# Kernel optimization log

Hardware: AMD Instinct MI355X
Metric: run time of the kernel (lower is better)

The kernel has to match this reference:

```python
import jax, jax.numpy as jnp
import numpy as np

K = 3          # kernel_size
P = K // 2     # padding


def setup_inputs() -> dict:
    key = jax.random.key(0)
    # [B, C, H, W]; first C-4 channels are per-class probabilities, last 4 are box offsets
    points = jax.random.normal(key, (4, 84, 512, 512), dtype=jnp.float32)
    return {"points": points}


def reference(points):
    # Peak (point) NMS: keep a pixel iff torch.argmax over its KxK window of
    # max-class-probability lands exactly on the window center.
    # torch.argmax returns the FIRST flat index attaining the max, so the center
    # survives iff it is strictly greater than every earlier (row-major) window
    # element and >= every later element.
    probs = jnp.max(points[:, :-4], axis=1)            # [B, H, W]
    B, H, W = probs.shape
    padded = jnp.pad(probs, ((0, 0), (P, P), (P, P)))  # zero pad, matches F.pad default
    center_idx = P * K + P
    mask = jnp.ones((B, H, W), dtype=bool)
    for di in range(K):                                # small fixed K*K loop (8 iters)
        for dj in range(K):
            idx = di * K + dj
            if idx == center_idx:
                continue
            nb = padded[:, di:di + H, dj:dj + W]       # neighbor value at this offset
            cmp = (probs > nb) if idx < center_idx else (probs >= nb)
            mask = mask & cmp
    # non-peaks zeroed across ALL channels, exactly like the zeros_like + scatter
    return points * mask[:, None, :, :].astype(points.dtype)
```

## Files before the change

### kernel.cpp

```cpp
#include <hip/hip_runtime.h>

#define BB 4
#define CC 84
#define CM 80
#define HH 512
#define WW 512
#define HWSZ (HH * WW)
#define PG (HWSZ / 4)
#define NCH 4
#define CPC (CM / NCH)

typedef float v4f __attribute__((ext_vector_type(4)));

static __device__ __forceinline__ v4f vmax4(v4f a, v4f b) {
    v4f r;
    r.x = fmaxf(a.x, b.x);
    r.y = fmaxf(a.y, b.y);
    r.z = fmaxf(a.z, b.z);
    r.w = fmaxf(a.w, b.w);
    return r;
}

__global__ __launch_bounds__(256) void partial_max_kernel(const float* __restrict__ pts,
                                                          float* __restrict__ partial) {
    int tid = blockIdx.x * blockDim.x + threadIdx.x;
    int pg  = tid & (PG - 1);
    int r   = tid >> 16;
    int chunk = r % NCH;
    int b     = r / NCH;

    const v4f* base = (const v4f*)pts + ((size_t)b * CC + chunk * CPC) * PG + pg;
    v4f m = __builtin_nontemporal_load(base);
#pragma unroll 5
    for (int c = 1; c < CPC; ++c) {
        v4f v = __builtin_nontemporal_load(base + (size_t)c * PG);
        m = vmax4(m, v);
    }
    ((v4f*)partial)[((size_t)chunk * BB + b) * PG + pg] = m;
}

__global__ __launch_bounds__(256) void fused_mask_kernel(const float* __restrict__ partial,
                                                         float* __restrict__ mask) {
    int tid = blockIdx.x * blockDim.x + threadIdx.x;
    int pg  = tid & (PG - 1);
    int b   = tid >> 16;
    int off = pg << 2;
    int h   = off >> 9;
    int w0  = off & (WW - 1);

    float rows[3][6];
#pragma unroll
    for (int r = 0; r < 3; ++r) {
        int hh = h + r - 1;
        bool hv = (hh >= 0) & (hh < HH);
#pragma unroll
        for (int ci = 0; ci < 6; ++ci) {
            int ww = w0 + ci - 1;
            bool wv = (ww >= 0) & (ww < WW);
            float v = 0.0f;
            if (hv & wv) {
                int pidx = hh * WW + ww;
                v = partial[(size_t)(0 * BB + b) * HWSZ + pidx];
#pragma unroll
                for (int ch = 1; ch < NCH; ++ch)
                    v = fmaxf(v, partial[(size_t)(ch * BB + b) * HWSZ + pidx]);
            }
            rows[r][ci] = v;
        }
    }

    v4f fm;
#pragma unroll
    for (int j = 0; j < 4; ++j) {
        float v = rows[1][j + 1];
        bool m = (v >  rows[0][j]) & (v >  rows[0][j + 1]) & (v >  rows[0][j + 2])
               & (v >  rows[1][j]) & (v >= rows[1][j + 2])
               & (v >= rows[2][j]) & (v >= rows[2][j + 1]) & (v >= rows[2][j + 2]);
        float f = m ? 1.0f : 0.0f;
        if (j == 0) fm.x = f;
        else if (j == 1) fm.y = f;
        else if (j == 2) fm.z = f;
        else fm.w = f;
    }
    ((v4f*)mask)[(size_t)b * PG + pg] = fm;
}

__global__ __launch_bounds__(256) void mul_kernel(const float* __restrict__ pts,
                                                  const float* __restrict__ mask,
                                                  float* __restrict__ out) {
    int gid = blockIdx.x;
    int c   = gid % CC;
    int pc  = gid / CC;
    int b   = pc >> 8;
    int pg  = ((pc & 255) << 8) + threadIdx.x;

    v4f m = ((const v4f*)mask)[(size_t)b * PG + pg];
    size_t idx = ((size_t)b * CC + c) * PG + pg;

    unsigned nz = (__float_as_uint(m.x) | __float_as_uint(m.y) |
                   __float_as_uint(m.z) | __float_as_uint(m.w));
    v4f o;
    if (nz) {
        v4f v = __builtin_nontemporal_load((const v4f*)pts + idx);
        o.x = v.x * m.x;
        o.y = v.y * m.y;
        o.z = v.z * m.z;
        o.w = v.w * m.w;
    } else {
        o.x = 0.f; o.y = 0.f; o.z = 0.f; o.w = 0.f;
    }
    __builtin_nontemporal_store(o, (v4f*)out + idx);
}

__global__ __launch_bounds__(256) void probs_kernel_fb(const float* __restrict__ pts,
                                                       float* __restrict__ probs) {
    int tid = blockIdx.x * blockDim.x + threadIdx.x;
    int pix = tid << 2;
    int b   = pix >> 18;
    int off = pix & (HWSZ - 1);
    const float4* base = (const float4*)(pts + (size_t)b * CC * HWSZ + off);
    float4 m = base[0];
#pragma unroll 4
    for (int c = 1; c < CM; ++c) {
        float4 v = base[c * (HWSZ / 4)];
        m.x = fmaxf(m.x, v.x); m.y = fmaxf(m.y, v.y);
        m.z = fmaxf(m.z, v.z); m.w = fmaxf(m.w, v.w);
    }
    ((float4*)probs)[tid] = m;
}

__global__ __launch_bounds__(256) void nms_mul_kernel_fb(const float* __restrict__ pts,
                                                         const float* __restrict__ probs,
                                                         float* __restrict__ out) {
    int tid = blockIdx.x * blockDim.x + threadIdx.x;
    int pix = tid << 2;
    int b   = pix >> 18;
    int off = pix & (HWSZ - 1);
    int h   = off >> 9;
    int w0  = off & (WW - 1);
    const float* pb = probs + b * HWSZ;
    float rows[3][6];
#pragma unroll
    for (int r = 0; r < 3; ++r) {
        int hh = h + r - 1;
        bool hv = (hh >= 0) & (hh < HH);
        const float* rp = pb + hh * WW;
#pragma unroll
        for (int ci = 0; ci < 6; ++ci) {
            int ww = w0 + ci - 1;
            bool wv = (ww >= 0) & (ww < WW);
            rows[r][ci] = (hv & wv) ? rp[ww] : 0.0f;
        }
    }
    float fm[4];
    bool any = false;
#pragma unroll
    for (int j = 0; j < 4; ++j) {
        float v = rows[1][j + 1];
        bool m = (v >  rows[0][j]) & (v >  rows[0][j + 1]) & (v >  rows[0][j + 2])
               & (v >  rows[1][j]) & (v >= rows[1][j + 2])
               & (v >= rows[2][j]) & (v >= rows[2][j + 1]) & (v >= rows[2][j + 2]);
        fm[j] = m ? 1.0f : 0.0f;
        any |= m;
    }
    size_t bo = (size_t)b * CC * HWSZ + off;
    const float4* src = (const float4*)(pts + bo);
    float4* dst = (float4*)(out + bo);
    if (any) {
#pragma unroll 4
        for (int c = 0; c < CC; ++c) {
            float4 v = src[c * (HWSZ / 4)];
            float4 o;
            o.x = v.x * fm[0]; o.y = v.y * fm[1];
            o.z = v.z * fm[2]; o.w = v.w * fm[3];
            dst[c * (HWSZ / 4)] = o;
        }
    } else {
        float4 z = make_float4(0.f, 0.f, 0.f, 0.f);
#pragma unroll 4
        for (int c = 0; c < CC; ++c) dst[c * (HWSZ / 4)] = z;
    }
}

extern "C" void kernel_launch(void* const* d_in, const int* in_sizes, int n_in,
                              void* d_out, int out_size, void* d_ws, size_t ws_size,
                              hipStream_t stream) {
    const float* pts = (const float*)d_in[0];
    float* out = (float*)d_out;
    float* ws  = (float*)d_ws;

    const size_t MB4 = (size_t)BB * HWSZ * sizeof(float);
    dim3 blk(256);
    dim3 grd_pg(BB * PG / 256);

    if (ws_size >= (NCH + 1) * MB4) {
        float* partial = ws;
        float* mask    = ws + (size_t)NCH * BB * HWSZ;
        partial_max_kernel<<<dim3(BB * NCH * PG / 256), blk, 0, stream>>>(pts, partial);
        fused_mask_kernel<<<grd_pg, blk, 0, stream>>>(partial, mask);
        mul_kernel<<<dim3(BB * CC * (PG / 256)), blk, 0, stream>>>(pts, mask, out);
    } else {
        float* probs = ws;
        probs_kernel_fb<<<grd_pg, blk, 0, stream>>>(pts, probs);
        nms_mul_kernel_fb<<<grd_pg, blk, 0, stream>>>(pts, probs, out);
    }
}
```

Baseline: 614.7 us.

## Fuse mask and multiply into one kernel; halve partial-max channel splits

Merges the stencil mask kernel and the per-channel multiply kernel into one kernel. Each block now computes the 3x3 peak mask itself and then streams 42 channels of points to the output, so the mask buffer is no longer written and re-read. The partial-max stage now splits channels into 2 chunks instead of 4, which shrinks the partial buffer and the stencil's reads. In exchange, the stencil is recomputed twice per pixel (once per half), and each thread runs a long serial channel loop with fewer blocks in flight.

```diff
diff --git a/kernel.cpp b/kernel.cpp
--- a/kernel.cpp
+++ b/kernel.cpp
@@ -7,8 +7,9 @@
 #define WW 512
 #define HWSZ (HH * WW)
 #define PG (HWSZ / 4)
-#define NCH 4
-#define CPC (CM / NCH)
+#define SPL 2
+#define CPS (CM / SPL)
+#define CPB (CC / SPL)
 
 typedef float v4f __attribute__((ext_vector_type(4)));
 
@@ -26,27 +27,33 @@
     int tid = blockIdx.x * blockDim.x + threadIdx.x;
     int pg  = tid & (PG - 1);
     int r   = tid >> 16;
-    int chunk = r % NCH;
-    int b     = r / NCH;
-
-    const v4f* base = (const v4f*)pts + ((size_t)b * CC + chunk * CPC) * PG + pg;
+    int half = r & 1;
+    int b    = r >> 1;
+
+    const v4f* base = (const v4f*)pts + ((size_t)b * CC + half * CPS) * PG + pg;
     v4f m = __builtin_nontemporal_load(base);
-#pragma unroll 5
-    for (int c = 1; c < CPC; ++c) {
+#pragma unroll 8
+    for (int c = 1; c < CPS; ++c) {
         v4f v = __builtin_nontemporal_load(base + (size_t)c * PG);
         m = vmax4(m, v);
     }
-    ((v4f*)partial)[((size_t)chunk * BB + b) * PG + pg] = m;
-}
-
-__global__ __launch_bounds__(256) void fused_mask_kernel(const float* __restrict__ partial,
-                                                         float* __restrict__ mask) {
-    int tid = blockIdx.x * blockDim.x + threadIdx.x;
-    int pg  = tid & (PG - 1);
-    int b   = tid >> 16;
-    int off = pg << 2;
-    int h   = off >> 9;
-    int w0  = off & (WW - 1);
+    ((v4f*)partial)[((size_t)half * BB + b) * PG + pg] = m;
+}
+
+__global__ __launch_bounds__(256) void nms_mul_kernel(const float* __restrict__ pts,
+                                                      const float* __restrict__ partial,
+                                                      float* __restrict__ out) {
+    int gid  = blockIdx.x;
+    int half = gid & 1;
+    int pc   = gid >> 1;
+    int b    = pc >> 8;
+    int pg   = ((pc & 255) << 8) + threadIdx.x;
+    int off  = pg << 2;
+    int h    = off >> 9;
+    int w0   = off & (WW - 1);
+
+    const float* p0 = partial + (size_t)b * HWSZ;
+    const float* p1 = partial + ((size_t)BB + b) * HWSZ;
 
     float rows[3][6];
 #pragma unroll
@@ -60,10 +67,7 @@
             float v = 0.0f;
             if (hv & wv) {
                 int pidx = hh * WW + ww;
-                v = partial[(size_t)(0 * BB + b) * HWSZ + pidx];
-#pragma unroll
-                for (int ch = 1; ch < NCH; ++ch)
-                    v = fmaxf(v, partial[(size_t)(ch * BB + b) * HWSZ + pidx]);
+                v = fmaxf(p0[pidx], p1[pidx]);
             }
             rows[r][ci] = v;
         }
@@ -82,34 +86,30 @@
         else if (j == 2) fm.z = f;
         else fm.w = f;
     }
-    ((v4f*)mask)[(size_t)b * PG + pg] = fm;
-}
-
-__global__ __launch_bounds__(256) void mul_kernel(const float* __restrict__ pts,
-                                                  const float* __restrict__ mask,
-                                                  float* __restrict__ out) {
-    int gid = blockIdx.x;
-    int c   = gid % CC;
-    int pc  = gid / CC;
-    int b   = pc >> 8;
-    int pg  = ((pc & 255) << 8) + threadIdx.x;
-
-    v4f m = ((const v4f*)mask)[(size_t)b * PG + pg];
-    size_t idx = ((size_t)b * CC + c) * PG + pg;
-
-    unsigned nz = (__float_as_uint(m.x) | __float_as_uint(m.y) |
-                   __float_as_uint(m.z) | __float_as_uint(m.w));
-    v4f o;
+    unsigned nz = (__float_as_uint(fm.x) | __float_as_uint(fm.y) |
+                   __float_as_uint(fm.z) | __float_as_uint(fm.w));
+
+    const v4f* src = (const v4f*)pts + ((size_t)b * CC + half * CPB) * PG + pg;
+    v4f*       dst = (v4f*)out       + ((size_t)b * CC + half * CPB) * PG + pg;
+
     if (nz) {
-        v4f v = __builtin_nontemporal_load((const v4f*)pts + idx);
-        o.x = v.x * m.x;
-        o.y = v.y * m.y;
-        o.z = v.z * m.z;
-        o.w = v.w * m.w;
+#pragma unroll 6
+        for (int c = 0; c < CPB; ++c) {
+            v4f v = __builtin_nontemporal_load(src + (size_t)c * PG);
+            v4f o;
+            o.x = v.x * fm.x;
+            o.y = v.y * fm.y;
+            o.z = v.z * fm.z;
+            o.w = v.w * fm.w;
+            __builtin_nontemporal_store(o, dst + (size_t)c * PG);
+        }
     } else {
-        o.x = 0.f; o.y = 0.f; o.z = 0.f; o.w = 0.f;
-    }
-    __builtin_nontemporal_store(o, (v4f*)out + idx);
+        v4f z;
+        z.x = 0.0f; z.y = 0.0f; z.z = 0.0f; z.w = 0.0f;
+#pragma unroll 6
+        for (int c = 0; c < CPB; ++c)
+            __builtin_nontemporal_store(z, dst + (size_t)c * PG);
+    }
 }
 
 __global__ __launch_bounds__(256) void probs_kernel_fb(const float* __restrict__ pts,
@@ -189,18 +189,16 @@
     float* out = (float*)d_out;
     float* ws  = (float*)d_ws;
 
-    const size_t MB4 = (size_t)BB * HWSZ * sizeof(float);
+    const size_t PSZ = (size_t)SPL * BB * HWSZ * sizeof(float);
     dim3 blk(256);
-    dim3 grd_pg(BB * PG / 256);
-
-    if (ws_size >= (NCH + 1) * MB4) {
+
+    if (ws_size >= PSZ) {
         float* partial = ws;
-        float* mask    = ws + (size_t)NCH * BB * HWSZ;
-        partial_max_kernel<<<dim3(BB * NCH * PG / 256), blk, 0, stream>>>(pts, partial);
-        fused_mask_kernel<<<grd_pg, blk, 0, stream>>>(partial, mask);
-        mul_kernel<<<dim3(BB * CC * (PG / 256)), blk, 0, stream>>>(pts, mask, out);
+        partial_max_kernel<<<dim3(BB * SPL * PG / 256), blk, 0, stream>>>(pts, partial);
+        nms_mul_kernel<<<dim3(BB * SPL * PG / 256), blk, 0, stream>>>(pts, partial, out);
     } else {
         float* probs = ws;
+        dim3 grd_pg(BB * PG / 256);
         probs_kernel_fb<<<grd_pg, blk, 0, stream>>>(pts, probs);
         nms_mul_kernel_fb<<<grd_pg, blk, 0, stream>>>(pts, probs, out);
     }
```

After: 817.5 us. +33.0%, slower.
